# Performance work log

Measured on AMD Instinct MI355X. Metric: run time of the kernel, lower is better.

Reference implementation:

```python
import jax, jax.numpy as jnp
import numpy as np

N = 100000
E = 3200000
NFEAT = 256
NHID = 128
NCLASS = 40
SCALE = 1.0


def setup_inputs() -> dict:
    key = jax.random.key(0)
    ks = jax.random.split(key, 8)
    x = jax.random.normal(ks[0], (N, NFEAT), dtype=jnp.float32)
    adj_row = jnp.sort(jax.random.randint(ks[1], (E,), 0, N, dtype=jnp.int32))
    adj_col = jax.random.randint(ks[2], (E,), 0, N, dtype=jnp.int32)
    adj_val = jax.random.uniform(ks[3], (E,), dtype=jnp.float32)
    # parameters (reset_parameters: weight ~ N(0,1), bias ~ N(-1,1) -> normal with mean -1? no:
    # bias.normal_(-stdv, stdv) with stdv=1 means mean=-1, std=1)
    W1 = jax.random.normal(ks[4], (NFEAT, NHID), dtype=jnp.float32)
    b1 = jax.random.normal(ks[5], (NHID,), dtype=jnp.float32) - 1.0
    W2 = jax.random.normal(ks[6], (NHID, NCLASS), dtype=jnp.float32)
    b2 = jax.random.normal(ks[7], (NCLASS,), dtype=jnp.float32) - 1.0
    return {"x": x, "adj_row": adj_row, "adj_col": adj_col, "adj_val": adj_val,
            "i": 0, "W1": W1, "b1": b1, "W2": W2, "b2": b2}


def spmm(row, col, val, dense):
    # adj @ dense where adj is sparse COO [N, N]
    gathered = val[:, None] * dense[col]          # [E, D]
    return jax.ops.segment_sum(gathered, row, num_segments=N)


def reference(x, adj_row, adj_col, adj_val, i, W1, b1, W2, b2):
    # layer 1: support = x @ W1; out = adj @ support + b1
    h = spmm(adj_row, adj_col, adj_val, x @ W1) + b1
    h = jax.nn.relu(h) * SCALE
    # dropout is identity (eval mode / training=False)
    # layer 2
    logits = spmm(adj_row, adj_col, adj_val, h @ W2) + b2
    return jax.nn.log_softmax(logits, axis=1)
```

## Files before the change

### kernel.cpp

```cpp
#include <hip/hip_runtime.h>
#include <hip/hip_bf16.h>
#include <math.h>


#define GCN_NFEAT 256
#define GCN_NHID  128
#define GCN_NCLASS 40

typedef __bf16 bf16_t;
typedef bf16_t bf16x8 __attribute__((ext_vector_type(8)));
typedef float  f32x4  __attribute__((ext_vector_type(4)));

static __device__ __forceinline__ unsigned short f2b(float f) {
    bf16_t b = (bf16_t)f;
    return *(unsigned short*)&b;
}
static __device__ __forceinline__ float blo(unsigned int u) {
    return __uint_as_float(u << 16);
}
static __device__ __forceinline__ float bhi(unsigned int u) {
    return __uint_as_float(u & 0xffff0000u);
}

__global__ __launch_bounds__(256) void k_row_ptr(
    const int* __restrict__ row, int* __restrict__ row_ptr, int n_rows, int n_edges)
{
    int r = blockIdx.x * blockDim.x + threadIdx.x;
    if (r > n_rows) return;
    int lo = 0, hi = n_edges;
    while (lo < hi) {
        int mid = (lo + hi) >> 1;
        if (row[mid] < r) lo = mid + 1; else hi = mid;
    }
    row_ptr[r] = lo;
}

__global__ __launch_bounds__(256) void k_prep_w1t(
    const float* __restrict__ w1, bf16_t* __restrict__ w1t)
{
    int idx = blockIdx.x * 256 + threadIdx.x;
    int c = idx & 127;
    int k = idx >> 7;
    w1t[(size_t)c * GCN_NFEAT + k] = (bf16_t)w1[(size_t)k * GCN_NHID + c];
}

__global__ __launch_bounds__(256) void k_prep_w2t(
    const float* __restrict__ w2, bf16_t* __restrict__ w2t)
{
    int idx = blockIdx.x * 256 + threadIdx.x;
    if (idx >= 48 * GCN_NHID) return;
    int c = idx / GCN_NHID;
    int k = idx - c * GCN_NHID;
    float v = (c < GCN_NCLASS) ? w2[(size_t)k * GCN_NCLASS + c] : 0.f;
    w2t[idx] = (bf16_t)v;
}

__global__ __launch_bounds__(256) void k_gemm1(
    const float* __restrict__ x, const bf16_t* __restrict__ w1t,
    bf16_t* __restrict__ out, int nrows)
{
    __shared__ __align__(16) bf16_t As[128][72];
    __shared__ __align__(16) bf16_t Bs[128][72];

    const int tid  = threadIdx.x;
    const int wave = tid >> 6, lane = tid & 63;
    const int wm = wave >> 1, wn = wave & 1;
    const int lm = lane & 15, quad = lane >> 4;
    const int r0 = blockIdx.x * 128;

    f32x4 acc[4][4] = {};

    for (int k0 = 0; k0 < GCN_NFEAT; k0 += 64) {
        {
            const int row = tid >> 1, half = tid & 1;
            const int gr = r0 + row;
            union { bf16_t b[32]; uint4 q[4]; } t;
            if (gr < nrows) {
                const float* p = x + (size_t)gr * GCN_NFEAT + k0 + half * 32;
#pragma unroll
                for (int i = 0; i < 8; i++) {
                    float4 v = ((const float4*)p)[i];
                    t.b[i*4+0] = (bf16_t)v.x; t.b[i*4+1] = (bf16_t)v.y;
                    t.b[i*4+2] = (bf16_t)v.z; t.b[i*4+3] = (bf16_t)v.w;
                }
            } else {
#pragma unroll
                for (int i = 0; i < 4; i++) t.q[i] = make_uint4(0,0,0,0);
            }
            uint4* dst = (uint4*)&As[row][half * 32];
#pragma unroll
            for (int i = 0; i < 4; i++) dst[i] = t.q[i];
        }
        {
            const int colc = tid >> 1, half = tid & 1;
            const uint4* src = (const uint4*)(w1t + (size_t)colc * GCN_NFEAT + k0 + half * 32);
            uint4* dst = (uint4*)&Bs[colc][half * 32];
#pragma unroll
            for (int i = 0; i < 4; i++) dst[i] = src[i];
        }
        __syncthreads();

#pragma unroll
        for (int ks = 0; ks < 2; ks++) {
            bf16x8 af[4], bfr[4];
#pragma unroll
            for (int i = 0; i < 4; i++)
                af[i] = *(const bf16x8*)&As[wm*64 + i*16 + lm][ks*32 + quad*8];
#pragma unroll
            for (int j = 0; j < 4; j++)
                bfr[j] = *(const bf16x8*)&Bs[wn*64 + j*16 + lm][ks*32 + quad*8];
#pragma unroll
            for (int i = 0; i < 4; i++)
#pragma unroll
                for (int j = 0; j < 4; j++)
                    acc[i][j] = __builtin_amdgcn_mfma_f32_16x16x32_bf16(
                        af[i], bfr[j], acc[i][j], 0, 0, 0);
        }
        __syncthreads();
    }

#pragma unroll
    for (int i = 0; i < 4; i++) {
#pragma unroll
        for (int reg = 0; reg < 4; reg++) {
            const int gr = r0 + wm*64 + i*16 + quad*4 + reg;
            if (gr < nrows) {
#pragma unroll
                for (int j = 0; j < 4; j++) {
                    const int gc = wn*64 + j*16 + lm;
                    out[(size_t)gr * GCN_NHID + gc] = (bf16_t)acc[i][j][reg];
                }
            }
        }
    }
}

__global__ __launch_bounds__(256) void k_spmm1(
    const int* __restrict__ row_ptr, const int* __restrict__ col,
    const float* __restrict__ val, const unsigned int* __restrict__ sup,
    const float* __restrict__ b1, unsigned int* __restrict__ h, int nrows)
{
    const int wid  = (blockIdx.x * blockDim.x + threadIdx.x) >> 6;
    const int lane = threadIdx.x & 63;
    if (wid >= nrows) return;
    const int e0 = row_ptr[wid];
    const int e1 = row_ptr[wid + 1];
    const int sub = lane & 15;

    float ax = 0.f, ay = 0.f;
    int e = e0;
    for (; e + 16 <= e1; e += 16) {
        const int   cv = col[e + sub];
        const float vv = val[e + sub];
#pragma unroll
        for (int j = 0; j < 16; j++) {
            const int   cj = __shfl(cv, j, 64);
            const float vj = __shfl(vv, j, 64);
            const unsigned int u = sup[(unsigned)(cj << 6) + lane];
            ax = fmaf(vj, blo(u), ax);
            ay = fmaf(vj, bhi(u), ay);
        }
    }
    for (; e < e1; e++) {
        const int c = col[e];
        const float v = val[e];
        const unsigned int u = sup[(unsigned)(c << 6) + lane];
        ax = fmaf(v, blo(u), ax);
        ay = fmaf(v, bhi(u), ay);
    }

    const float2 bb = *(const float2*)(b1 + lane * 2);
    const float ox = fmaxf(ax + bb.x, 0.f);
    const float oy = fmaxf(ay + bb.y, 0.f);
    h[(unsigned)(wid << 6) + lane] = (unsigned int)f2b(ox) | ((unsigned int)f2b(oy) << 16);
}

__global__ __launch_bounds__(256) void k_gemm2(
    const bf16_t* __restrict__ h, const bf16_t* __restrict__ w2t,
    bf16_t* __restrict__ out, int nrows)
{
    __shared__ __align__(16) bf16_t As[128][136];
    __shared__ __align__(16) bf16_t Bs[48][136];

    const int tid  = threadIdx.x;
    const int wave = tid >> 6, lane = tid & 63;
    const int lm = lane & 15, quad = lane >> 4;
    const int r0 = blockIdx.x * 128;

    {
        const int row = tid >> 1, half = tid & 1;
        const int gr = r0 + row;
        uint4* dst = (uint4*)&As[row][half * 64];
        if (gr < nrows) {
            const uint4* src = (const uint4*)(h + (size_t)gr * GCN_NHID + half * 64);
#pragma unroll
            for (int i = 0; i < 8; i++) dst[i] = src[i];
        } else {
#pragma unroll
            for (int i = 0; i < 8; i++) dst[i] = make_uint4(0,0,0,0);
        }
    }
    for (int idx = tid; idx < 48 * 16; idx += 256) {
        const int c = idx >> 4, seg = idx & 15;
        ((uint4*)&Bs[c][0])[seg] = ((const uint4*)(w2t + (size_t)c * GCN_NHID))[seg];
    }
    __syncthreads();

    f32x4 acc[2][3] = {};
#pragma unroll
    for (int ks = 0; ks < 4; ks++) {
        bf16x8 af[2], bfr[3];
#pragma unroll
        for (int i = 0; i < 2; i++)
            af[i] = *(const bf16x8*)&As[wave*32 + i*16 + lm][ks*32 + quad*8];
#pragma unroll
        for (int j = 0; j < 3; j++)
            bfr[j] = *(const bf16x8*)&Bs[j*16 + lm][ks*32 + quad*8];
#pragma unroll
        for (int i = 0; i < 2; i++)
#pragma unroll
            for (int j = 0; j < 3; j++)
                acc[i][j] = __builtin_amdgcn_mfma_f32_16x16x32_bf16(
                    af[i], bfr[j], acc[i][j], 0, 0, 0);
    }

#pragma unroll
    for (int i = 0; i < 2; i++) {
#pragma unroll
        for (int reg = 0; reg < 4; reg++) {
            const int gr = r0 + wave*32 + i*16 + quad*4 + reg;
            if (gr < nrows) {
#pragma unroll
                for (int j = 0; j < 3; j++) {
                    const int gc = j*16 + lm;
                    if (gc < GCN_NCLASS)
                        out[(size_t)gr * GCN_NCLASS + gc] = (bf16_t)acc[i][j][reg];
                }
            }
        }
    }
}

__global__ __launch_bounds__(256) void k_spmm2_lsm(
    const int* __restrict__ row_ptr, const int* __restrict__ col,
    const float* __restrict__ val, const unsigned int* __restrict__ sup2,
    const float* __restrict__ b2, float* __restrict__ out, int nrows)
{
    const int wid  = (blockIdx.x * blockDim.x + threadIdx.x) >> 6;
    const int lane = threadIdx.x & 63;
    const int g    = lane / 20;
    const int li   = lane - g * 20;
    const int r    = wid * 3 + g;
    const bool active = (g < 3) && (r < nrows);

    int e0 = 0, e1 = 0;
    if (active) { e0 = row_ptr[r]; e1 = row_ptr[r + 1]; }

    float ax = 0.f, ay = 0.f;
    int e = e0;
    for (; e + 3 < e1; e += 4) {
        const int c0 = col[e],   c1 = col[e+1], c2 = col[e+2], c3 = col[e+3];
        const float v0 = val[e], v1 = val[e+1], v2 = val[e+2], v3 = val[e+3];
        const unsigned int u0 = sup2[(unsigned)(c0 * 20) + li];
        const unsigned int u1 = sup2[(unsigned)(c1 * 20) + li];
        const unsigned int u2 = sup2[(unsigned)(c2 * 20) + li];
        const unsigned int u3 = sup2[(unsigned)(c3 * 20) + li];
        ax = fmaf(v0, blo(u0), ax); ay = fmaf(v0, bhi(u0), ay);
        ax = fmaf(v1, blo(u1), ax); ay = fmaf(v1, bhi(u1), ay);
        ax = fmaf(v2, blo(u2), ax); ay = fmaf(v2, bhi(u2), ay);
        ax = fmaf(v3, blo(u3), ax); ay = fmaf(v3, bhi(u3), ay);
    }
    for (; e < e1; e++) {
        const unsigned int u = sup2[(unsigned)(col[e] * 20) + li];
        const float v = val[e];
        ax = fmaf(v, blo(u), ax); ay = fmaf(v, bhi(u), ay);
    }

    float l0 = -INFINITY, l1 = -INFINITY;
    if (active) {
        l0 = ax + b2[li * 2];
        l1 = ay + b2[li * 2 + 1];
    }

    float m = fmaxf(l0, l1);
#pragma unroll
    for (int off = 16; off >= 1; off >>= 1) {
        const float t = __shfl_down(m, off, 64);
        if (li + off < 20) m = fmaxf(m, t);
    }
    m = __shfl(m, g * 20, 64);

    float s = active ? (__expf(l0 - m) + __expf(l1 - m)) : 0.f;
#pragma unroll
    for (int off = 16; off >= 1; off >>= 1) {
        const float t = __shfl_down(s, off, 64);
        if (li + off < 20) s += t;
    }
    s = __shfl(s, g * 20, 64);

    if (active) {
        const float lse = m + __logf(s);
        float* p = out + (size_t)r * GCN_NCLASS + li * 2;
        p[0] = l0 - lse;
        p[1] = l1 - lse;
    }
}

extern "C" void kernel_launch(void* const* d_in, const int* in_sizes, int n_in,
                              void* d_out, int out_size, void* d_ws, size_t ws_size,
                              hipStream_t stream)
{
    const float* x       = (const float*)d_in[0];
    const int*   adj_row = (const int*)  d_in[1];
    const int*   adj_col = (const int*)  d_in[2];
    const float* adj_val = (const float*)d_in[3];
    const float* W1 = (const float*)d_in[5];
    const float* b1 = (const float*)d_in[6];
    const float* W2 = (const float*)d_in[7];
    const float* b2 = (const float*)d_in[8];
    float* out = (float*)d_out;

    const int N = in_sizes[0] / GCN_NFEAT;
    const int E = in_sizes[1];

    char* ws = (char*)d_ws;
    size_t off = 0;
    int* row_ptr = (int*)(ws + off);
    off += (((size_t)(N + 1) * sizeof(int)) + 1023) & ~(size_t)1023;
    bf16_t* w1t = (bf16_t*)(ws + off);
    off += ((size_t)GCN_NHID * GCN_NFEAT * 2 + 1023) & ~(size_t)1023;
    bf16_t* w2t = (bf16_t*)(ws + off);
    off += ((size_t)48 * GCN_NHID * 2 + 1023) & ~(size_t)1023;
    bf16_t* sup1 = (bf16_t*)(ws + off);
    off += ((size_t)N * GCN_NHID * 2 + 1023) & ~(size_t)1023;
    bf16_t* h = (bf16_t*)(ws + off);
    bf16_t* sup2 = sup1;

    k_row_ptr<<<(N + 1 + 255) / 256, 256, 0, stream>>>(adj_row, row_ptr, N, E);
    k_prep_w1t<<<GCN_NHID * GCN_NFEAT / 256, 256, 0, stream>>>(W1, w1t);
    k_prep_w2t<<<(48 * GCN_NHID + 255) / 256, 256, 0, stream>>>(W2, w2t);
    k_gemm1<<<(N + 127) / 128, 256, 0, stream>>>(x, w1t, sup1, N);
    k_spmm1<<<(N + 3) / 4, 256, 0, stream>>>(row_ptr, adj_col, adj_val,
                                             (const unsigned int*)sup1, b1,
                                             (unsigned int*)h, N);
    k_gemm2<<<(N + 127) / 128, 256, 0, stream>>>(h, w2t, sup2, N);
    const int nw2 = (N + 2) / 3;
    k_spmm2_lsm<<<(nw2 + 3) / 4, 256, 0, stream>>>(row_ptr, adj_col, adj_val,
                                                   (const unsigned int*)sup2, b2, out, N);
}
```

Baseline: 417.3 us.

## Split edges across half-waves in SpMM1 and one-row-per-wave SpMM2

SpMM1 now has each half-wave handle alternate edges with 8-byte loads (4 bf16 per lane), then combine the halves with a cross-lane xor shuffle. This halves the per-edge gather instructions and doubles memory-level parallelism. SpMM2 changes from three rows per wave to one row per wave, with three 20-lane groups taking interleaved edges and a shuffle reduction at the end. Index loads use nontemporal hints, which adds shuffle and reduction overhead and leaves idle lanes in SpMM2.

```diff
diff --git a/kernel.cpp b/kernel.cpp
--- a/kernel.cpp
+++ b/kernel.cpp
@@ -137,42 +137,71 @@
 
 __global__ __launch_bounds__(256) void k_spmm1(
     const int* __restrict__ row_ptr, const int* __restrict__ col,
-    const float* __restrict__ val, const unsigned int* __restrict__ sup,
-    const float* __restrict__ b1, unsigned int* __restrict__ h, int nrows)
+    const float* __restrict__ val, const unsigned long long* __restrict__ sup,
+    const float* __restrict__ b1, unsigned long long* __restrict__ h, int nrows)
 {
     const int wid  = (blockIdx.x * blockDim.x + threadIdx.x) >> 6;
     const int lane = threadIdx.x & 63;
     if (wid >= nrows) return;
     const int e0 = row_ptr[wid];
     const int e1 = row_ptr[wid + 1];
-    const int sub = lane & 15;
-
-    float ax = 0.f, ay = 0.f;
+    const int eg = lane >> 5;
+    const int li = lane & 31;
+
+    float a0 = 0.f, a1 = 0.f, a2 = 0.f, a3 = 0.f;
+
     int e = e0;
     for (; e + 16 <= e1; e += 16) {
-        const int   cv = col[e + sub];
-        const float vv = val[e + sub];
-#pragma unroll
-        for (int j = 0; j < 16; j++) {
-            const int   cj = __shfl(cv, j, 64);
-            const float vj = __shfl(vv, j, 64);
-            const unsigned int u = sup[(unsigned)(cj << 6) + lane];
-            ax = fmaf(vj, blo(u), ax);
-            ay = fmaf(vj, bhi(u), ay);
-        }
-    }
-    for (; e < e1; e++) {
-        const int c = col[e];
+        const int   cv = __builtin_nontemporal_load(&col[e + (lane & 15)]);
+        const float vv = __builtin_nontemporal_load(&val[e + (lane & 15)]);
+#pragma unroll
+        for (int s = 0; s < 8; s++) {
+            const int   cj = __shfl(cv, 2 * s + eg, 64);
+            const float vj = __shfl(vv, 2 * s + eg, 64);
+            const unsigned long long u = sup[((unsigned)cj << 5) + li];
+            const unsigned int ux = (unsigned int)u;
+            const unsigned int uy = (unsigned int)(u >> 32);
+            a0 = fmaf(vj, blo(ux), a0); a1 = fmaf(vj, bhi(ux), a1);
+            a2 = fmaf(vj, blo(uy), a2); a3 = fmaf(vj, bhi(uy), a3);
+        }
+    }
+    for (; e + 2 <= e1; e += 2) {
+        const int   c = col[e + eg];
+        const float v = val[e + eg];
+        const unsigned long long u = sup[((unsigned)c << 5) + li];
+        const unsigned int ux = (unsigned int)u;
+        const unsigned int uy = (unsigned int)(u >> 32);
+        a0 = fmaf(v, blo(ux), a0); a1 = fmaf(v, bhi(ux), a1);
+        a2 = fmaf(v, blo(uy), a2); a3 = fmaf(v, bhi(uy), a3);
+    }
+    if (e < e1) {
+        const int   c = col[e];
         const float v = val[e];
-        const unsigned int u = sup[(unsigned)(c << 6) + lane];
-        ax = fmaf(v, blo(u), ax);
-        ay = fmaf(v, bhi(u), ay);
-    }
-
-    const float2 bb = *(const float2*)(b1 + lane * 2);
-    const float ox = fmaxf(ax + bb.x, 0.f);
-    const float oy = fmaxf(ay + bb.y, 0.f);
-    h[(unsigned)(wid << 6) + lane] = (unsigned int)f2b(ox) | ((unsigned int)f2b(oy) << 16);
+        if (eg == 0) {
+            const unsigned long long u = sup[((unsigned)c << 5) + li];
+            const unsigned int ux = (unsigned int)u;
+            const unsigned int uy = (unsigned int)(u >> 32);
+            a0 = fmaf(v, blo(ux), a0); a1 = fmaf(v, bhi(ux), a1);
+            a2 = fmaf(v, blo(uy), a2); a3 = fmaf(v, bhi(uy), a3);
+        }
+    }
+
+    a0 += __shfl_xor(a0, 32, 64);
+    a1 += __shfl_xor(a1, 32, 64);
+    a2 += __shfl_xor(a2, 32, 64);
+    a3 += __shfl_xor(a3, 32, 64);
+
+    if (eg == 0) {
+        const float4 bb = *(const float4*)(b1 + li * 4);
+        const float o0 = fmaxf(a0 + bb.x, 0.f);
+        const float o1 = fmaxf(a1 + bb.y, 0.f);
+        const float o2 = fmaxf(a2 + bb.z, 0.f);
+        const float o3 = fmaxf(a3 + bb.w, 0.f);
+        const unsigned long long pk =
+            (unsigned long long)((unsigned int)f2b(o0) | ((unsigned int)f2b(o1) << 16)) |
+            ((unsigned long long)((unsigned int)f2b(o2) | ((unsigned int)f2b(o3) << 16)) << 32);
+        __builtin_nontemporal_store(pk, &h[((unsigned)wid << 5) + li]);
+    }
 }
 
 __global__ __launch_bounds__(256) void k_gemm2(
@@ -248,61 +277,74 @@
 {
     const int wid  = (blockIdx.x * blockDim.x + threadIdx.x) >> 6;
     const int lane = threadIdx.x & 63;
-    const int g    = lane / 20;
-    const int li   = lane - g * 20;
-    const int r    = wid * 3 + g;
-    const bool active = (g < 3) && (r < nrows);
-
-    int e0 = 0, e1 = 0;
-    if (active) { e0 = row_ptr[r]; e1 = row_ptr[r + 1]; }
+    if (wid >= nrows) return;
+    int g = lane / 20;
+    const int li = lane - g * 20;
+    if (g > 2) g = 2;
+
+    const int e0 = row_ptr[wid];
+    const int e1 = row_ptr[wid + 1];
 
     float ax = 0.f, ay = 0.f;
     int e = e0;
-    for (; e + 3 < e1; e += 4) {
-        const int c0 = col[e],   c1 = col[e+1], c2 = col[e+2], c3 = col[e+3];
-        const float v0 = val[e], v1 = val[e+1], v2 = val[e+2], v3 = val[e+3];
-        const unsigned int u0 = sup2[(unsigned)(c0 * 20) + li];
-        const unsigned int u1 = sup2[(unsigned)(c1 * 20) + li];
-        const unsigned int u2 = sup2[(unsigned)(c2 * 20) + li];
-        const unsigned int u3 = sup2[(unsigned)(c3 * 20) + li];
-        ax = fmaf(v0, blo(u0), ax); ay = fmaf(v0, bhi(u0), ay);
-        ax = fmaf(v1, blo(u1), ax); ay = fmaf(v1, bhi(u1), ay);
-        ax = fmaf(v2, blo(u2), ax); ay = fmaf(v2, bhi(u2), ay);
-        ax = fmaf(v3, blo(u3), ax); ay = fmaf(v3, bhi(u3), ay);
-    }
-    for (; e < e1; e++) {
-        const unsigned int u = sup2[(unsigned)(col[e] * 20) + li];
-        const float v = val[e];
-        ax = fmaf(v, blo(u), ax); ay = fmaf(v, bhi(u), ay);
-    }
-
+    for (; e + 24 <= e1; e += 24) {
+        const int   idx = (lane < 24) ? lane : 0;
+        const int   cv = __builtin_nontemporal_load(&col[e + idx]);
+        const float vv = __builtin_nontemporal_load(&val[e + idx]);
+#pragma unroll
+        for (int s = 0; s < 8; s++) {
+            const int   cj = __shfl(cv, s * 3 + g, 64);
+            const float vj = __shfl(vv, s * 3 + g, 64);
+            const unsigned int u = sup2[(unsigned)cj * 20 + li];
+            ax = fmaf(vj, blo(u), ax);
+            ay = fmaf(vj, bhi(u), ay);
+        }
+    }
+    for (int et = e + g; et < e1; et += 3) {
+        const int   c = col[et];
+        const float v = val[et];
+        const unsigned int u = sup2[(unsigned)c * 20 + li];
+        ax = fmaf(v, blo(u), ax);
+        ay = fmaf(v, bhi(u), ay);
+    }
+
+    {
+        const float tx20 = __shfl_down(ax, 20, 64);
+        const float tx40 = __shfl_down(ax, 40, 64);
+        const float ty20 = __shfl_down(ay, 20, 64);
+        const float ty40 = __shfl_down(ay, 40, 64);
+        ax = ax + tx20 + tx40;
+        ay = ay + ty20 + ty40;
+    }
+
+    const bool owner = (lane < 20);
     float l0 = -INFINITY, l1 = -INFINITY;
-    if (active) {
-        l0 = ax + b2[li * 2];
-        l1 = ay + b2[li * 2 + 1];
+    if (owner) {
+        const float2 bb = *(const float2*)(b2 + li * 2);
+        l0 = ax + bb.x;
+        l1 = ay + bb.y;
     }
 
     float m = fmaxf(l0, l1);
 #pragma unroll
     for (int off = 16; off >= 1; off >>= 1) {
         const float t = __shfl_down(m, off, 64);
-        if (li + off < 20) m = fmaxf(m, t);
-    }
-    m = __shfl(m, g * 20, 64);
-
-    float s = active ? (__expf(l0 - m) + __expf(l1 - m)) : 0.f;
+        if (owner && li + off < 20) m = fmaxf(m, t);
+    }
+    m = __shfl(m, 0, 64);
+
+    float s = owner ? (__expf(l0 - m) + __expf(l1 - m)) : 0.f;
 #pragma unroll
     for (int off = 16; off >= 1; off >>= 1) {
         const float t = __shfl_down(s, off, 64);
-        if (li + off < 20) s += t;
-    }
-    s = __shfl(s, g * 20, 64);
-
-    if (active) {
+        if (owner && li + off < 20) s += t;
+    }
+    s = __shfl(s, 0, 64);
+
+    if (owner) {
         const float lse = m + __logf(s);
-        float* p = out + (size_t)r * GCN_NCLASS + li * 2;
-        p[0] = l0 - lse;
-        p[1] = l1 - lse;
+        float2 o = make_float2(l0 - lse, l1 - lse);
+        *(float2*)(out + (size_t)wid * GCN_NCLASS + li * 2) = o;
     }
 }
 
@@ -341,10 +383,9 @@
     k_prep_w2t<<<(48 * GCN_NHID + 255) / 256, 256, 0, stream>>>(W2, w2t);
     k_gemm1<<<(N + 127) / 128, 256, 0, stream>>>(x, w1t, sup1, N);
     k_spmm1<<<(N + 3) / 4, 256, 0, stream>>>(row_ptr, adj_col, adj_val,
-                                             (const unsigned int*)sup1, b1,
-                                             (unsigned int*)h, N);
+                                             (const unsigned long long*)sup1, b1,
+                                             (unsigned long long*)h, N);
     k_gemm2<<<(N + 127) / 128, 256, 0, stream>>>(h, w2t, sup2, N);
-    const int nw2 = (N + 2) / 3;
-    k_spmm2_lsm<<<(nw2 + 3) / 4, 256, 0, stream>>>(row_ptr, adj_col, adj_val,
-                                                   (const unsigned int*)sup2, b2, out, N);
-}
+    k_spmm2_lsm<<<(N + 3) / 4, 256, 0, stream>>>(row_ptr, adj_col, adj_val,
+                                                 (const unsigned int*)sup2, b2, out, N);
+}
```

Result: slower. 434.2 us (+4.0%).

## Partition layer-1 support into column panels and split SpMM by panel

Applied to the files above, without the earlier changes.

The first GEMM now writes its output as eight 16-column panels, each stored contiguously across all rows. The first SpMM launches one block group per panel, so each pass gathers only a 32-byte slice per neighbor. The aim is for a panel's working set (about 3.2 MB) to stay in cache rather than spilling to HBM on random gathers. Each wave handles 8 edges at once with 8 lanes per edge, then reduces with cross-lane shuffles. The costs are reading col/val eight times over (with nontemporal loads), smaller per-lane gathers, and extra block launches.

```diff
diff --git a/kernel.cpp b/kernel.cpp
--- a/kernel.cpp
+++ b/kernel.cpp
@@ -127,8 +127,8 @@
             if (gr < nrows) {
 #pragma unroll
                 for (int j = 0; j < 4; j++) {
-                    const int gc = wn*64 + j*16 + lm;
-                    out[(size_t)gr * GCN_NHID + gc] = (bf16_t)acc[i][j][reg];
+                    const int p = wn*4 + j;
+                    out[((size_t)p * nrows + gr) * 16 + lm] = (bf16_t)acc[i][j][reg];
                 }
             }
         }
@@ -137,42 +137,56 @@
 
 __global__ __launch_bounds__(256) void k_spmm1(
     const int* __restrict__ row_ptr, const int* __restrict__ col,
-    const float* __restrict__ val, const unsigned int* __restrict__ sup,
+    const float* __restrict__ val, const unsigned int* __restrict__ sup1p,
     const float* __restrict__ b1, unsigned int* __restrict__ h, int nrows)
 {
-    const int wid  = (blockIdx.x * blockDim.x + threadIdx.x) >> 6;
-    const int lane = threadIdx.x & 63;
-    if (wid >= nrows) return;
-    const int e0 = row_ptr[wid];
-    const int e1 = row_ptr[wid + 1];
-    const int sub = lane & 15;
+    const int p     = blockIdx.x & 7;
+    const int chunk = blockIdx.x >> 3;
+    const int wave  = threadIdx.x >> 6;
+    const int lane  = threadIdx.x & 63;
+    const int r     = chunk * 4 + wave;
+    if (r >= nrows) return;
+
+    const int eg = lane >> 3;
+    const int li = lane & 7;
+    const unsigned int* sp = sup1p + (size_t)p * nrows * 8;
+
+    const int e0 = row_ptr[r];
+    const int e1 = row_ptr[r + 1];
 
     float ax = 0.f, ay = 0.f;
     int e = e0;
-    for (; e + 16 <= e1; e += 16) {
-        const int   cv = col[e + sub];
-        const float vv = val[e + sub];
-#pragma unroll
-        for (int j = 0; j < 16; j++) {
-            const int   cj = __shfl(cv, j, 64);
-            const float vj = __shfl(vv, j, 64);
-            const unsigned int u = sup[(unsigned)(cj << 6) + lane];
+    for (; e + 32 <= e1; e += 32) {
+        const int   cv = __builtin_nontemporal_load(&col[e + (lane & 31)]);
+        const float vv = __builtin_nontemporal_load(&val[e + (lane & 31)]);
+#pragma unroll
+        for (int s = 0; s < 4; s++) {
+            const int   cj = __shfl(cv, s * 8 + eg, 64);
+            const float vj = __shfl(vv, s * 8 + eg, 64);
+            const unsigned int u = sp[(unsigned)cj * 8u + li];
             ax = fmaf(vj, blo(u), ax);
             ay = fmaf(vj, bhi(u), ay);
         }
     }
-    for (; e < e1; e++) {
-        const int c = col[e];
-        const float v = val[e];
-        const unsigned int u = sup[(unsigned)(c << 6) + lane];
+    for (int k = e + eg; k < e1; k += 8) {
+        const int   c = col[k];
+        const float v = val[k];
+        const unsigned int u = sp[(unsigned)c * 8u + li];
         ax = fmaf(v, blo(u), ax);
         ay = fmaf(v, bhi(u), ay);
     }
 
-    const float2 bb = *(const float2*)(b1 + lane * 2);
-    const float ox = fmaxf(ax + bb.x, 0.f);
-    const float oy = fmaxf(ay + bb.y, 0.f);
-    h[(unsigned)(wid << 6) + lane] = (unsigned int)f2b(ox) | ((unsigned int)f2b(oy) << 16);
+    ax += __shfl_xor(ax, 8, 64);  ay += __shfl_xor(ay, 8, 64);
+    ax += __shfl_xor(ax, 16, 64); ay += __shfl_xor(ay, 16, 64);
+    ax += __shfl_xor(ax, 32, 64); ay += __shfl_xor(ay, 32, 64);
+
+    if (lane < 8) {
+        const float2 bb = *(const float2*)(b1 + p * 16 + li * 2);
+        const float ox = fmaxf(ax + bb.x, 0.f);
+        const float oy = fmaxf(ay + bb.y, 0.f);
+        const unsigned int pk = (unsigned int)f2b(ox) | ((unsigned int)f2b(oy) << 16);
+        h[(unsigned)r * 64u + (unsigned)p * 8u + li] = pk;
+    }
 }
 
 __global__ __launch_bounds__(256) void k_gemm2(
@@ -331,18 +345,19 @@
     off += ((size_t)GCN_NHID * GCN_NFEAT * 2 + 1023) & ~(size_t)1023;
     bf16_t* w2t = (bf16_t*)(ws + off);
     off += ((size_t)48 * GCN_NHID * 2 + 1023) & ~(size_t)1023;
-    bf16_t* sup1 = (bf16_t*)(ws + off);
+    bf16_t* sup1p = (bf16_t*)(ws + off);
     off += ((size_t)N * GCN_NHID * 2 + 1023) & ~(size_t)1023;
     bf16_t* h = (bf16_t*)(ws + off);
-    bf16_t* sup2 = sup1;
+    bf16_t* sup2 = sup1p;
 
     k_row_ptr<<<(N + 1 + 255) / 256, 256, 0, stream>>>(adj_row, row_ptr, N, E);
     k_prep_w1t<<<GCN_NHID * GCN_NFEAT / 256, 256, 0, stream>>>(W1, w1t);
     k_prep_w2t<<<(48 * GCN_NHID + 255) / 256, 256, 0, stream>>>(W2, w2t);
-    k_gemm1<<<(N + 127) / 128, 256, 0, stream>>>(x, w1t, sup1, N);
-    k_spmm1<<<(N + 3) / 4, 256, 0, stream>>>(row_ptr, adj_col, adj_val,
-                                             (const unsigned int*)sup1, b1,
-                                             (unsigned int*)h, N);
+    k_gemm1<<<(N + 127) / 128, 256, 0, stream>>>(x, w1t, sup1p, N);
+    const int nblk1 = ((N + 3) / 4) * 8;
+    k_spmm1<<<nblk1, 256, 0, stream>>>(row_ptr, adj_col, adj_val,
+                                       (const unsigned int*)sup1p, b1,
+                                       (unsigned int*)h, N);
     k_gemm2<<<(N + 127) / 128, 256, 0, stream>>>(h, w2t, sup2, N);
     const int nw2 = (N + 2) / 3;
     k_spmm2_lsm<<<(nw2 + 3) / 4, 256, 0, stream>>>(row_ptr, adj_col, adj_val,
```

Measured after the change: 705.9 us. 69.2% more time.
